# Performance work log

Hardware: AMD Instinct MI355X
Metric: run time of the kernel (lower is better)

## Reference

```python
import jax, jax.numpy as jnp
import numpy as np

N, M, K, C, FF, H, OUT = 20000, 80000, 48, 64, 256, 4, 64


def _lin(x, w, b):
    return x @ w.T + b


def _bn(x, g, b, eps=1e-5):
    mu = x.mean(0)
    var = x.var(0)
    return (x - mu) * jax.lax.rsqrt(var + eps) * g + b


def setup_inputs() -> dict:
    key = jax.random.key(0)
    ks = jax.random.split(key, 24)
    voxel_features = jax.random.normal(ks[0], (M, C), jnp.float32)
    voxel_coords = jax.random.normal(ks[1], (M, 3), jnp.float32)
    query_coords = jax.random.normal(ks[2], (N, 3), jnp.float32)
    idx = jax.random.randint(ks[3], (N, K), 0, M)
    drop = jax.random.uniform(ks[4], (N, K)) < 0.1
    drop = drop.at[:, 0].set(False)  # keep >=1 valid key per query
    key_indices = jnp.where(drop, -1, idx)
    s = 0.05
    p = lambda i, shp: jax.random.normal(ks[i], shp, jnp.float32) * s
    return {
        "voxel_features": voxel_features,
        "voxel_coords": voxel_coords,
        "query_coords": query_coords,
        "key_indices": key_indices,
        "q_w": p(5, (C, 3)), "q_b": p(6, (C,)),
        "kpos_w": p(7, (C, 3)), "kpos_b": p(8, (C,)),
        "in_w": p(9, (3 * C, C)), "in_b": p(10, (3 * C,)),
        "out_w": p(11, (C, C)), "out_b": p(12, (C,)),
        "lin1_w": p(13, (FF, C)), "lin1_b": p(14, (FF,)),
        "lin2_w": p(15, (C, FF)), "lin2_b": p(16, (C,)),
        "norm_g": jnp.ones((C,), jnp.float32), "norm_b": jnp.zeros((C,), jnp.float32),
        "outl_w": p(17, (OUT, C)), "outl_b": p(18, (OUT,)),
        "obn_g": jnp.ones((OUT,), jnp.float32), "obn_b": jnp.zeros((OUT,), jnp.float32),
    }


def reference(voxel_features, voxel_coords, query_coords, key_indices,
              q_w, q_b, kpos_w, kpos_b, in_w, in_b, out_w, out_b,
              lin1_w, lin1_b, lin2_w, lin2_b, norm_g, norm_b,
              outl_w, outl_b, obn_g, obn_b):
    hd = C // H
    mask = key_indices < 0                      # (N,K) padded keys
    safe = jnp.where(mask, 0, key_indices)
    key_feats = voxel_features[safe]            # (N,K,C) hash-gather
    key_coords = voxel_coords[safe]             # (N,K,3)
    # query positional projection
    q_feat = jax.nn.relu(_lin(query_coords, q_w, q_b))          # (N,C)
    # relative coords + key positional conv1d(kernel=1) == linear on coord dim
    rel = key_coords - query_coords[:, None, :]                  # (N,K,3)
    key_feats = key_feats + jax.nn.relu(_lin(rel, kpos_w, kpos_b))
    # multihead attention, query length 1 per voxel
    Wq, Wk, Wv = jnp.split(in_w, 3, axis=0)
    bq, bk, bv = jnp.split(in_b, 3)
    q = (_lin(q_feat, Wq, bq) / jnp.sqrt(jnp.float32(hd))).reshape(N, H, hd)
    k = _lin(key_feats, Wk, bk).reshape(N, K, H, hd)
    v = _lin(key_feats, Wv, bv).reshape(N, K, H, hd)
    scores = jnp.einsum('nhd,nkhd->nhk', q, k)
    scores = jnp.where(mask[:, None, :], -jnp.inf, scores)
    attn = jax.nn.softmax(scores, axis=-1)
    ctx = jnp.einsum('nhk,nkhd->nhd', attn, v).reshape(N, C)
    att = _lin(ctx, out_w, out_b)                                # (N,C)
    # FFN + residual
    x = att + _lin(jax.nn.relu(_lin(att, lin1_w, lin1_b)), lin2_w, lin2_b)
    x = _bn(x, norm_g, norm_b)
    # output layer: Linear -> BN -> ReLU
    x = jax.nn.relu(_bn(_lin(x, outl_w, outl_b), obn_g, obn_b))
    return x
```

## Files before the change

### kernel.cpp

```cpp
#include <hip/hip_runtime.h>
#include <math.h>

#define N_Q 20000
#define KK 48
#define CC 64
#define FFD 256

#define TW_WOT   0
#define TW_WVT   4096
#define TW_L1B   8192
#define TW_L2B   16384
#define TW_OLB   24576
#define TW_QB    26624
#define TW_KB    28672
#define ST_OFF   32768
#define M_OFF    33024
#define VF_OFF   2593024

typedef short bf16x8 __attribute__((ext_vector_type(8)));
typedef float f32x4  __attribute__((ext_vector_type(4)));

__device__ __forceinline__ unsigned f2bf(float f) {
    unsigned u = __float_as_uint(f);
    return (u + 0x7fffu + ((u >> 16) & 1u)) >> 16;
}
__device__ __forceinline__ unsigned pk2(float a, float b) {
    return f2bf(a) | (f2bf(b) << 16);
}
__device__ __forceinline__ float bflo(unsigned u) { return __uint_as_float(u << 16); }
__device__ __forceinline__ float bfhi(unsigned u) { return __uint_as_float(u & 0xffff0000u); }
__device__ __forceinline__ bf16x8 ldfrag(const unsigned short* p) {
    return *(const bf16x8*)p;
}

__global__ void prep_all(const float* __restrict__ in_w,
                         const float* __restrict__ out_w,
                         const float* __restrict__ lin1_w,
                         const float* __restrict__ lin2_w,
                         const float* __restrict__ outl_w,
                         const float* __restrict__ vfeat,
                         float* __restrict__ tw,
                         unsigned short* __restrict__ vfeat_bf,
                         float* __restrict__ stats)
{
    int t = blockIdx.x * 256 + threadIdx.x;
    unsigned* twu = (unsigned*)tw;
    if (t < 1280000) {
        float4 v = ((const float4*)vfeat)[t];
        uint2 p; p.x = pk2(v.x, v.y); p.y = pk2(v.z, v.w);
        ((uint2*)vfeat_bf)[t] = p;
    }
    if (t < 256) stats[t] = 0.0f;
    if (t < 4096) {
        int c = t >> 6, j = t & 63;
        tw[TW_WOT + j*64 + c] = out_w[c*64 + j];
    } else if (t < 8192) {
        if (t < 6144) {
            int p = t - 4096;
            int j2 = p & 3, lane = (p >> 2) & 63, nb = (p >> 8) & 3, ks = p >> 10;
            int nn = nb*16 + (lane & 15), k = ks*32 + (lane >> 4)*8 + 2*j2;
            twu[TW_WVT + p] = pk2(in_w[(128 + nn)*64 + k], in_w[(128 + nn)*64 + k + 1]);
        }
    } else if (t < 16384) {
        int p = t - 8192;
        int j2 = p & 3, lane = (p >> 2) & 63, nb = (p >> 8) & 15, ks = p >> 12;
        int n = nb*16 + (lane & 15), k = ks*32 + (lane >> 4)*8 + 2*j2;
        twu[TW_L1B + p] = pk2(lin1_w[n*64 + k], lin1_w[n*64 + k + 1]);
    } else if (t < 24576) {
        int p = t - 16384;
        int j2 = p & 3, lane = (p >> 2) & 63, nb = (p >> 8) & 3, ks = p >> 10;
        int n = nb*16 + (lane & 15), k = ks*32 + (lane >> 4)*8 + 2*j2;
        twu[TW_L2B + p] = pk2(lin2_w[n*256 + k], lin2_w[n*256 + k + 1]);
    } else if (t < 26624) {
        int p = t - 24576;
        int j2 = p & 3, lane = (p >> 2) & 63, nb = (p >> 8) & 3, ks = p >> 10;
        int n = nb*16 + (lane & 15), k = ks*32 + (lane >> 4)*8 + 2*j2;
        twu[TW_OLB + p] = pk2(outl_w[n*64 + k], outl_w[n*64 + k + 1]);
    } else if (t < 28672) {
        int p = t - 26624;
        int j2 = p & 3, lane = (p >> 2) & 63, nb = (p >> 8) & 3, ks = p >> 10;
        int n = nb*16 + (lane & 15), k = ks*32 + (lane >> 4)*8 + 2*j2;
        twu[TW_QB + p] = pk2(in_w[n*64 + k], in_w[n*64 + k + 1]);
    } else if (t < 32768) {
        int p = t - 28672;
        int j2 = p & 3, lane = (p >> 2) & 63, nb = (p >> 8) & 3, h = p >> 10;
        int j = nb*16 + (lane & 15), k = (lane >> 4)*8 + 2*j2;
        unsigned u = 0;
        if (k < 16)
            u = pk2(in_w[(64 + h*16 + k)*64 + j], in_w[(64 + h*16 + k + 1)*64 + j]);
        twu[TW_KB + p] = u;
    }
}

__global__ __launch_bounds__(256) void m_kernel(
    const float* __restrict__ qcoord, const float* __restrict__ q_w,
    const float* __restrict__ q_b, const float* __restrict__ in_b,
    const float* __restrict__ tw, unsigned short* __restrict__ M_all)
{
    __shared__ __align__(16) unsigned short sQF[80*72];
    __shared__ __align__(16) unsigned short sQ[80*72];
    int t = threadIdx.x, base = blockIdx.x * 80;
    int colq = (t*4) & 63;
    float qwv[12];
    #pragma unroll
    for (int j = 0; j < 12; ++j) qwv[j] = q_w[colq*3 + j];
    float4 qb4 = *(const float4*)&q_b[colq];
    #pragma unroll
    for (int i = 0; i < 5; ++i) {
        int e = i*1024 + t*4, r = e >> 6, n = base + r;
        float c0 = qcoord[n*3], c1 = qcoord[n*3+1], c2 = qcoord[n*3+2];
        float f0 = fmaxf(fmaf(qwv[2],  c2, fmaf(qwv[1],  c1, fmaf(qwv[0], c0, qb4.x))), 0.f);
        float f1 = fmaxf(fmaf(qwv[5],  c2, fmaf(qwv[4],  c1, fmaf(qwv[3], c0, qb4.y))), 0.f);
        float f2 = fmaxf(fmaf(qwv[8],  c2, fmaf(qwv[7],  c1, fmaf(qwv[6], c0, qb4.z))), 0.f);
        float f3 = fmaxf(fmaf(qwv[11], c2, fmaf(qwv[10], c1, fmaf(qwv[9], c0, qb4.w))), 0.f);
        uint2 p; p.x = pk2(f0, f1); p.y = pk2(f2, f3);
        *(uint2*)&sQF[r*72 + colq] = p;
    }
    int w = t >> 6, lane = t & 63, l16 = lane & 15, quad = lane >> 4;
    const unsigned* QB = (const unsigned*)(tw + TW_QB);
    const unsigned* KB = (const unsigned*)(tw + TW_KB);
    bf16x8 qbf[2], kbf[4];
    #pragma unroll
    for (int ks = 0; ks < 2; ++ks)
        qbf[ks] = ldfrag((const unsigned short*)&QB[((ks*4 + w)*64 + lane)*4]);
    #pragma unroll
    for (int nb = 0; nb < 4; ++nb)
        kbf[nb] = ldfrag((const unsigned short*)&KB[((w*4 + nb)*64 + lane)*4]);
    __syncthreads();

    int cq = w*16 + l16;
    float bq = in_b[cq];
    #pragma unroll
    for (int mb = 0; mb < 5; ++mb) {
        bf16x8 a0 = ldfrag(&sQF[(mb*16 + l16)*72 + quad*8]);
        bf16x8 a1 = ldfrag(&sQF[(mb*16 + l16)*72 + 32 + quad*8]);
        f32x4 acc = {0.f, 0.f, 0.f, 0.f};
        acc = __builtin_amdgcn_mfma_f32_16x16x32_bf16(a0, qbf[0], acc, 0, 0, 0);
        acc = __builtin_amdgcn_mfma_f32_16x16x32_bf16(a1, qbf[1], acc, 0, 0, 0);
        #pragma unroll
        for (int reg = 0; reg < 4; ++reg) {
            int row = mb*16 + quad*4 + reg;
            sQ[row*72 + cq] = (unsigned short)f2bf((acc[reg] + bq) * 0.25f);
        }
    }
    #pragma unroll
    for (int mb = 0; mb < 5; ++mb) {
        bf16x8 a = {0,0,0,0,0,0,0,0};
        if (quad < 2) a = ldfrag(&sQ[(mb*16 + l16)*72 + w*16 + quad*8]);
        f32x4 acc[4];
        #pragma unroll
        for (int nb = 0; nb < 4; ++nb) {
            f32x4 z = {0.f, 0.f, 0.f, 0.f};
            acc[nb] = __builtin_amdgcn_mfma_f32_16x16x32_bf16(a, kbf[nb], z, 0, 0, 0);
        }
        #pragma unroll
        for (int nb = 0; nb < 4; ++nb)
            #pragma unroll
            for (int reg = 0; reg < 4; ++reg) {
                int r = base + mb*16 + quad*4 + reg, j = nb*16 + l16;
                M_all[(size_t)r*256 + w*64 + j] = (unsigned short)f2bf(acc[nb][reg]);
            }
    }
}

__global__ __launch_bounds__(64, 4) void attn_kernel(
    const unsigned short* __restrict__ vfeat_bf, const float* __restrict__ vcoord,
    const float* __restrict__ qcoord, const int* __restrict__ kidx,
    const float* __restrict__ kpos_w, const float* __restrict__ kpos_b,
    const float* __restrict__ in_b, const float* __restrict__ out_b,
    const float* __restrict__ tw, const unsigned short* __restrict__ M_all,
    float* __restrict__ att_out)
{
    __shared__ __align__(16) unsigned short skf[KK*72];
    __shared__ __align__(16) float sctx[64];
    int n = blockIdx.x, c = threadIdx.x;
    int l16 = c & 15, quad = c >> 4;

    const unsigned short* Mrow = M_all + (size_t)n*256 + (l16 & 3)*64 + quad*8;
    bf16x8 mf0 = ldfrag(Mrow);
    bf16x8 mf1 = ldfrag(Mrow + 32);
    const unsigned* VBu = (const unsigned*)(tw + TW_WVT);
    bf16x8 wv[2][4];
    #pragma unroll
    for (int ks = 0; ks < 2; ++ks)
        #pragma unroll
        for (int nb = 0; nb < 4; ++nb)
            wv[ks][nb] = ldfrag((const unsigned short*)&VBu[((ks*4 + nb)*64 + c)*4]);

    float qc0 = qcoord[n*3+0], qc1 = qcoord[n*3+1], qc2 = qcoord[n*3+2];

    int kread = c < 48 ? c : 47;
    int idxv = kidx[(size_t)n*KK + kread];
    int sfe = idxv < 0 ? 0 : idxv;
    float rl0 = vcoord[sfe*3+0] - qc0;
    float rl1 = vcoord[sfe*3+1] - qc1;
    float rl2 = vcoord[sfe*3+2] - qc2;

    float4 wA  = *(const float4*)(kpos_w + 12*l16 + 0);
    float4 wB  = *(const float4*)(kpos_w + 12*l16 + 4);
    float4 wC  = *(const float4*)(kpos_w + 12*l16 + 8);
    float4 kb4 = *(const float4*)(kpos_b + 4*l16);

    uint2 fv[12];
    #pragma unroll
    for (int i = 0; i < 12; ++i) {
        int row = 4*i + quad;
        int si = __shfl(idxv, row);
        si = si < 0 ? 0 : si;
        fv[i] = *(const uint2*)(vfeat_bf + (size_t)si*64 + 4*l16);
    }
    #pragma unroll
    for (int i = 0; i < 12; ++i) {
        int row = 4*i + quad;
        float rr0 = __shfl(rl0, row), rr1 = __shfl(rl1, row), rr2 = __shfl(rl2, row);
        float g0 = bflo(fv[i].x), g1 = bfhi(fv[i].x);
        float g2 = bflo(fv[i].y), g3 = bfhi(fv[i].y);
        g0 += fmaxf(fmaf(wA.x, rr0, fmaf(wA.y, rr1, fmaf(wA.z, rr2, kb4.x))), 0.0f);
        g1 += fmaxf(fmaf(wA.w, rr0, fmaf(wB.x, rr1, fmaf(wB.y, rr2, kb4.y))), 0.0f);
        g2 += fmaxf(fmaf(wB.z, rr0, fmaf(wB.w, rr1, fmaf(wC.x, rr2, kb4.z))), 0.0f);
        g3 += fmaxf(fmaf(wC.y, rr0, fmaf(wC.z, rr1, fmaf(wC.w, rr2, kb4.w))), 0.0f);
        uint2 p; p.x = pk2(g0, g1); p.y = pk2(g2, g3);
        *(uint2*)&skf[row*72 + 4*l16] = p;
    }

    unsigned long long vm = __ballot(c < 48 && idxv >= 0);
    bf16x8 a0s[3], a1s[3];
    float S[3][4];
    #pragma unroll
    for (int mb = 0; mb < 3; ++mb) {
        a0s[mb] = ldfrag(&skf[(mb*16 + l16)*72 + quad*8]);
        a1s[mb] = ldfrag(&skf[(mb*16 + l16)*72 + 32 + quad*8]);
        f32x4 acc = {0.f, 0.f, 0.f, 0.f};
        acc = __builtin_amdgcn_mfma_f32_16x16x32_bf16(a0s[mb], mf0, acc, 0, 0, 0);
        acc = __builtin_amdgcn_mfma_f32_16x16x32_bf16(a1s[mb], mf1, acc, 0, 0, 0);
        #pragma unroll
        for (int r = 0; r < 4; ++r) {
            int kk = mb*16 + quad*4 + r;
            S[mb][r] = ((vm >> kk) & 1ull) ? acc[r] : -1e30f;
        }
    }

    float mx = S[0][0];
    #pragma unroll
    for (int mb = 0; mb < 3; ++mb)
        #pragma unroll
        for (int r = 0; r < 4; ++r) mx = fmaxf(mx, S[mb][r]);
    mx = fmaxf(mx, __shfl_xor(mx, 16));
    mx = fmaxf(mx, __shfl_xor(mx, 32));
    float p[3][4], es = 0.f;
    #pragma unroll
    for (int mb = 0; mb < 3; ++mb)
        #pragma unroll
        for (int r = 0; r < 4; ++r) { p[mb][r] = __expf(S[mb][r] - mx); es += p[mb][r]; }
    es += __shfl_xor(es, 16);
    es += __shfl_xor(es, 32);
    float rinv = 1.0f / es;
    #pragma unroll
    for (int mb = 0; mb < 3; ++mb)
        #pragma unroll
        for (int r = 0; r < 4; ++r) p[mb][r] *= rinv;

    float cacc0 = 0.f, cacc1 = 0.f, cacc2 = 0.f, cacc3 = 0.f;
    #pragma unroll
    for (int mb = 0; mb < 3; ++mb) {
        f32x4 av[4];
        #pragma unroll
        for (int nb = 0; nb < 4; ++nb) {
            f32x4 z = {0.f, 0.f, 0.f, 0.f};
            z = __builtin_amdgcn_mfma_f32_16x16x32_bf16(a0s[mb], wv[0][nb], z, 0, 0, 0);
            av[nb] = __builtin_amdgcn_mfma_f32_16x16x32_bf16(a1s[mb], wv[1][nb], z, 0, 0, 0);
        }
        #pragma unroll
        for (int r = 0; r < 4; ++r) {
            float pv = p[mb][r];
            float p0 = __shfl(pv, quad*16 + 0);
            float p1 = __shfl(pv, quad*16 + 1);
            float p2 = __shfl(pv, quad*16 + 2);
            float p3 = __shfl(pv, quad*16 + 3);
            cacc0 = fmaf(p0, av[0][r], cacc0);
            cacc1 = fmaf(p1, av[1][r], cacc1);
            cacc2 = fmaf(p2, av[2][r], cacc2);
            cacc3 = fmaf(p3, av[3][r], cacc3);
        }
    }
    cacc0 += __shfl_xor(cacc0, 16); cacc0 += __shfl_xor(cacc0, 32);
    cacc1 += __shfl_xor(cacc1, 16); cacc1 += __shfl_xor(cacc1, 32);
    cacc2 += __shfl_xor(cacc2, 16); cacc2 += __shfl_xor(cacc2, 32);
    cacc3 += __shfl_xor(cacc3, 16); cacc3 += __shfl_xor(cacc3, 32);
    float cv = quad == 0 ? cacc0 : quad == 1 ? cacc1 : quad == 2 ? cacc2 : cacc3;
    cv += in_b[128 + c];
    sctx[c] = cv;

    const float* WoT = tw + TW_WOT;
    float att = out_b[c];
    #pragma unroll 8
    for (int j = 0; j < 64; ++j)
        att = fmaf(sctx[j], WoT[j*64 + c], att);
    att_out[(size_t)n*64 + c] = att;
}

__global__ __launch_bounds__(256) void ffn_kernel(
    const float* __restrict__ tw, const float* __restrict__ lin1_b,
    const float* __restrict__ lin2_b, float* __restrict__ att_y,
    float* __restrict__ sum1, float* __restrict__ sumsq1)
{
    __shared__ __align__(16) unsigned short sA[80*72];
    __shared__ __align__(16) unsigned short sH[80*264];
    int t = threadIdx.x, base = blockIdx.x * 80;
    #pragma unroll
    for (int i = 0; i < 5; ++i) {
        int e = i*1024 + t*4, r = e >> 6, col = e & 63;
        float4 v = *(const float4*)&att_y[(size_t)(base + r)*64 + col];
        uint2 p; p.x = pk2(v.x, v.y); p.y = pk2(v.z, v.w);
        *(uint2*)&sA[r*72 + col] = p;
    }
    int w = t >> 6, lane = t & 63, l16 = lane & 15, quad = lane >> 4;
    const unsigned* L1B = (const unsigned*)(tw + TW_L1B);
    const unsigned* L2B = (const unsigned*)(tw + TW_L2B);
    bf16x8 b1f[2][4], b2f[8];
    #pragma unroll
    for (int ks = 0; ks < 2; ++ks)
        #pragma unroll
        for (int nb = 0; nb < 4; ++nb)
            b1f[ks][nb] = ldfrag((const unsigned short*)&L1B[((ks*16 + w*4 + nb)*64 + lane)*4]);
    #pragma unroll
    for (int ks = 0; ks < 8; ++ks)
        b2f[ks] = ldfrag((const unsigned short*)&L2B[((ks*4 + w)*64 + lane)*4]);
    __syncthreads();

    #pragma unroll
    for (int mb = 0; mb < 5; ++mb) {
        bf16x8 a0 = ldfrag(&sA[(mb*16 + l16)*72 + quad*8]);
        bf16x8 a1 = ldfrag(&sA[(mb*16 + l16)*72 + 32 + quad*8]);
        #pragma unroll
        for (int nb = 0; nb < 4; ++nb) {
            f32x4 acc = {0.f, 0.f, 0.f, 0.f};
            acc = __builtin_amdgcn_mfma_f32_16x16x32_bf16(a0, b1f[0][nb], acc, 0, 0, 0);
            acc = __builtin_amdgcn_mfma_f32_16x16x32_bf16(a1, b1f[1][nb], acc, 0, 0, 0);
            int f = w*64 + nb*16 + l16;
            float bias = lin1_b[f];
            #pragma unroll
            for (int reg = 0; reg < 4; ++reg) {
                int row = mb*16 + quad*4 + reg;
                sH[row*264 + f] = (unsigned short)f2bf(fmaxf(acc[reg] + bias, 0.0f));
            }
        }
    }
    __syncthreads();

    int c = w*16 + l16;
    float lb2 = lin2_b[c];
    float s = 0.f, ss = 0.f;
    #pragma unroll
    for (int mb = 0; mb < 5; ++mb) {
        f32x4 acc = {0.f, 0.f, 0.f, 0.f};
        #pragma unroll
        for (int ks = 0; ks < 8; ++ks) {
            bf16x8 a = ldfrag(&sH[(mb*16 + l16)*264 + ks*32 + quad*8]);
            acc = __builtin_amdgcn_mfma_f32_16x16x32_bf16(a, b2f[ks], acc, 0, 0, 0);
        }
        #pragma unroll
        for (int reg = 0; reg < 4; ++reg) {
            int r = base + mb*16 + quad*4 + reg;
            float y = att_y[(size_t)r*64 + c] + lb2 + acc[reg];
            att_y[(size_t)r*64 + c] = y;
            s += y; ss = fmaf(y, y, ss);
        }
    }
    s  += __shfl_xor(s, 16);  s  += __shfl_xor(s, 32);
    ss += __shfl_xor(ss, 16); ss += __shfl_xor(ss, 32);
    if (lane < 16) {
        atomicAdd(&sum1[c], s);
        atomicAdd(&sumsq1[c], ss);
    }
}

__global__ __launch_bounds__(256) void linout_kernel(
    const float* __restrict__ tw, const float* __restrict__ outl_b,
    const float* __restrict__ norm_g, const float* __restrict__ norm_b,
    const float* __restrict__ sum1, const float* __restrict__ sumsq1,
    const float* __restrict__ y, float* __restrict__ z_out,
    float* __restrict__ sum2, float* __restrict__ sumsq2)
{
    __shared__ __align__(16) unsigned short sX[80*72];
    int t = threadIdx.x, base = blockIdx.x * 80;
    int colq = (t*4) & 63;
    const float invN = 1.0f / 20000.0f;
    float4 sm = *(const float4*)&sum1[colq];
    float4 sq = *(const float4*)&sumsq1[colq];
    float4 g  = *(const float4*)&norm_g[colq];
    float4 bb = *(const float4*)&norm_b[colq];
    float mu0 = sm.x*invN, mu1 = sm.y*invN, mu2 = sm.z*invN, mu3 = sm.w*invN;
    float a0 = g.x / sqrtf(fmaf(-mu0, mu0, sq.x*invN) + 1e-5f);
    float a1 = g.y / sqrtf(fmaf(-mu1, mu1, sq.y*invN) + 1e-5f);
    float a2 = g.z / sqrtf(fmaf(-mu2, mu2, sq.z*invN) + 1e-5f);
    float a3 = g.w / sqrtf(fmaf(-mu3, mu3, sq.w*invN) + 1e-5f);
    float b0 = fmaf(-mu0, a0, bb.x), b1 = fmaf(-mu1, a1, bb.y);
    float b2 = fmaf(-mu2, a2, bb.z), b3 = fmaf(-mu3, a3, bb.w);
    #pragma unroll
    for (int i = 0; i < 5; ++i) {
        int e = i*1024 + t*4, r = e >> 6;
        float4 v = *(const float4*)&y[(size_t)(base + r)*64 + colq];
        uint2 p;
        p.x = pk2(fmaf(v.x, a0, b0), fmaf(v.y, a1, b1));
        p.y = pk2(fmaf(v.z, a2, b2), fmaf(v.w, a3, b3));
        *(uint2*)&sX[r*72 + colq] = p;
    }
    int w = t >> 6, lane = t & 63, l16 = lane & 15, quad = lane >> 4;
    const unsigned* OLB = (const unsigned*)(tw + TW_OLB);
    bf16x8 obf[2];
    #pragma unroll
    for (int ks = 0; ks < 2; ++ks)
        obf[ks] = ldfrag((const unsigned short*)&OLB[((ks*4 + w)*64 + lane)*4]);
    __syncthreads();

    int co = w*16 + l16;
    float ob = outl_b[co];
    float s = 0.f, ss = 0.f;
    #pragma unroll
    for (int mb = 0; mb < 5; ++mb) {
        bf16x8 x0 = ldfrag(&sX[(mb*16 + l16)*72 + quad*8]);
        bf16x8 x1 = ldfrag(&sX[(mb*16 + l16)*72 + 32 + quad*8]);
        f32x4 acc = {0.f, 0.f, 0.f, 0.f};
        acc = __builtin_amdgcn_mfma_f32_16x16x32_bf16(x0, obf[0], acc, 0, 0, 0);
        acc = __builtin_amdgcn_mfma_f32_16x16x32_bf16(x1, obf[1], acc, 0, 0, 0);
        #pragma unroll
        for (int reg = 0; reg < 4; ++reg) {
            int r = base + mb*16 + quad*4 + reg;
            float zv = acc[reg] + ob;
            z_out[(size_t)r*64 + co] = zv;
            s += zv; ss = fmaf(zv, zv, ss);
        }
    }
    s  += __shfl_xor(s, 16);  s  += __shfl_xor(s, 32);
    ss += __shfl_xor(ss, 16); ss += __shfl_xor(ss, 32);
    if (lane < 16) {
        atomicAdd(&sum2[co], s);
        atomicAdd(&sumsq2[co], ss);
    }
}

__global__ void final_kernel(float* __restrict__ z,
    const float* __restrict__ sum2, const float* __restrict__ sumsq2,
    const float* __restrict__ obn_g, const float* __restrict__ obn_b)
{
    int i = blockIdx.x*blockDim.x + threadIdx.x;
    if (i >= N_Q*64/4) return;
    int o4 = (i*4) & 63;
    float4 sm = *(const float4*)&sum2[o4];
    float4 sq = *(const float4*)&sumsq2[o4];
    float4 g  = *(const float4*)&obn_g[o4];
    float4 b  = *(const float4*)&obn_b[o4];
    const float invN = 1.0f / 20000.0f;
    float mux = sm.x*invN, muy = sm.y*invN, muz = sm.z*invN, muw = sm.w*invN;
    float ax = g.x / sqrtf(fmaf(-mux, mux, sq.x*invN) + 1e-5f);
    float ay = g.y / sqrtf(fmaf(-muy, muy, sq.y*invN) + 1e-5f);
    float az = g.z / sqrtf(fmaf(-muz, muz, sq.z*invN) + 1e-5f);
    float aw = g.w / sqrtf(fmaf(-muw, muw, sq.w*invN) + 1e-5f);
    float4 v = ((float4*)z)[i];
    v.x = fmaxf(fmaf(v.x - mux, ax, b.x), 0.0f);
    v.y = fmaxf(fmaf(v.y - muy, ay, b.y), 0.0f);
    v.z = fmaxf(fmaf(v.z - muz, az, b.z), 0.0f);
    v.w = fmaxf(fmaf(v.w - muw, aw, b.w), 0.0f);
    ((float4*)z)[i] = v;
}

extern "C" void kernel_launch(void* const* d_in, const int* in_sizes, int n_in,
                              void* d_out, int out_size, void* d_ws, size_t ws_size,
                              hipStream_t stream)
{
    const float* vfeat  = (const float*)d_in[0];
    const float* vcoord = (const float*)d_in[1];
    const float* qcoord = (const float*)d_in[2];
    const int*   kidx   = (const int*)d_in[3];
    const float* q_w    = (const float*)d_in[4];
    const float* q_b    = (const float*)d_in[5];
    const float* kpos_w = (const float*)d_in[6];
    const float* kpos_b = (const float*)d_in[7];
    const float* in_w   = (const float*)d_in[8];
    const float* in_b   = (const float*)d_in[9];
    const float* out_w  = (const float*)d_in[10];
    const float* out_b  = (const float*)d_in[11];
    const float* lin1_w = (const float*)d_in[12];
    const float* lin1_b = (const float*)d_in[13];
    const float* lin2_w = (const float*)d_in[14];
    const float* lin2_b = (const float*)d_in[15];
    const float* norm_g = (const float*)d_in[16];
    const float* norm_b = (const float*)d_in[17];
    const float* outl_w = (const float*)d_in[18];
    const float* outl_b = (const float*)d_in[19];
    const float* obn_g  = (const float*)d_in[20];
    const float* obn_b  = (const float*)d_in[21];

    float* ws = (float*)d_ws;
    float* tw = ws;
    float* stats = ws + ST_OFF;
    float* sum1 = stats, *sumsq1 = stats + 64, *sum2 = stats + 128, *sumsq2 = stats + 192;
    unsigned short* M_all = (unsigned short*)(ws + M_OFF);
    unsigned short* vfeat_bf = (unsigned short*)(ws + VF_OFF);
    float* xd = (float*)d_out;

    prep_all<<<5120, 256, 0, stream>>>(in_w, out_w, lin1_w, lin2_w, outl_w,
                                       vfeat, tw, vfeat_bf, stats);
    m_kernel<<<250, 256, 0, stream>>>(qcoord, q_w, q_b, in_b, tw, M_all);
    attn_kernel<<<N_Q, 64, 0, stream>>>(vfeat_bf, vcoord, qcoord, kidx, kpos_w, kpos_b,
                                        in_b, out_b, tw, M_all, xd);
    ffn_kernel<<<250, 256, 0, stream>>>(tw, lin1_b, lin2_b, xd, sum1, sumsq1);
    linout_kernel<<<250, 256, 0, stream>>>(tw, outl_b, norm_g, norm_b, sum1, sumsq1,
                                           xd, xd, sum2, sumsq2);
    final_kernel<<<1250, 256, 0, stream>>>(xd, sum2, sumsq2, obn_g, obn_b);
}
```

Before: 185.6 us.

## Move out-projection into FFN kernel as MFMA GEMM and pack two queries per attn block

The per-query scalar out_proj loop (64x64 FMAs reading a transposed fp32 weight) is removed from the attention kernel. The attention kernel now writes ctx, and the FFN kernel runs out_proj as a bf16 MFMA GEMM over 80-row tiles, keeping att in registers for the residual. The attention kernel also handles two queries per 128-thread block, halving the block count. This trades fp32 precision on out_proj for bf16 and adds LDS reuse of the sH buffer in the FFN kernel.

```diff
diff --git a/kernel.cpp b/kernel.cpp
--- a/kernel.cpp
+++ b/kernel.cpp
@@ -6,7 +6,7 @@
 #define CC 64
 #define FFD 256
 
-#define TW_WOT   0
+#define TW_WOB   0
 #define TW_WVT   4096
 #define TW_L1B   8192
 #define TW_L2B   16384
@@ -52,8 +52,12 @@
     }
     if (t < 256) stats[t] = 0.0f;
     if (t < 4096) {
-        int c = t >> 6, j = t & 63;
-        tw[TW_WOT + j*64 + c] = out_w[c*64 + j];
+        if (t < 2048) {
+            int p = t;
+            int j2 = p & 3, lane = (p >> 2) & 63, nb = (p >> 8) & 3, ks = p >> 10;
+            int nn = nb*16 + (lane & 15), k = ks*32 + (lane >> 4)*8 + 2*j2;
+            twu[TW_WOB + p] = pk2(out_w[nn*64 + k], out_w[nn*64 + k + 1]);
+        }
     } else if (t < 8192) {
         if (t < 6144) {
             int p = t - 4096;
@@ -163,29 +167,30 @@
     }
 }
 
-__global__ __launch_bounds__(64, 4) void attn_kernel(
+__global__ __launch_bounds__(128, 4) void attn_kernel(
     const unsigned short* __restrict__ vfeat_bf, const float* __restrict__ vcoord,
     const float* __restrict__ qcoord, const int* __restrict__ kidx,
     const float* __restrict__ kpos_w, const float* __restrict__ kpos_b,
-    const float* __restrict__ in_b, const float* __restrict__ out_b,
+    const float* __restrict__ in_b,
     const float* __restrict__ tw, const unsigned short* __restrict__ M_all,
-    float* __restrict__ att_out)
-{
-    __shared__ __align__(16) unsigned short skf[KK*72];
-    __shared__ __align__(16) float sctx[64];
-    int n = blockIdx.x, c = threadIdx.x;
+    float* __restrict__ ctx_out)
+{
+    __shared__ __align__(16) unsigned short skf2[2][KK*72];
+    int wv = threadIdx.x >> 6, c = threadIdx.x & 63;
+    int n = blockIdx.x * 2 + wv;
+    unsigned short* skf = skf2[wv];
     int l16 = c & 15, quad = c >> 4;
 
     const unsigned short* Mrow = M_all + (size_t)n*256 + (l16 & 3)*64 + quad*8;
     bf16x8 mf0 = ldfrag(Mrow);
     bf16x8 mf1 = ldfrag(Mrow + 32);
     const unsigned* VBu = (const unsigned*)(tw + TW_WVT);
-    bf16x8 wv[2][4];
+    bf16x8 wvf[2][4];
     #pragma unroll
     for (int ks = 0; ks < 2; ++ks)
         #pragma unroll
         for (int nb = 0; nb < 4; ++nb)
-            wv[ks][nb] = ldfrag((const unsigned short*)&VBu[((ks*4 + nb)*64 + c)*4]);
+            wvf[ks][nb] = ldfrag((const unsigned short*)&VBu[((ks*4 + nb)*64 + c)*4]);
 
     float qc0 = qcoord[n*3+0], qc1 = qcoord[n*3+1], qc2 = qcoord[n*3+2];
 
@@ -267,8 +272,8 @@
         #pragma unroll
         for (int nb = 0; nb < 4; ++nb) {
             f32x4 z = {0.f, 0.f, 0.f, 0.f};
-            z = __builtin_amdgcn_mfma_f32_16x16x32_bf16(a0s[mb], wv[0][nb], z, 0, 0, 0);
-            av[nb] = __builtin_amdgcn_mfma_f32_16x16x32_bf16(a1s[mb], wv[1][nb], z, 0, 0, 0);
+            z = __builtin_amdgcn_mfma_f32_16x16x32_bf16(a0s[mb], wvf[0][nb], z, 0, 0, 0);
+            av[nb] = __builtin_amdgcn_mfma_f32_16x16x32_bf16(a1s[mb], wvf[1][nb], z, 0, 0, 0);
         }
         #pragma unroll
         for (int r = 0; r < 4; ++r) {
@@ -289,35 +294,34 @@
     cacc3 += __shfl_xor(cacc3, 16); cacc3 += __shfl_xor(cacc3, 32);
     float cv = quad == 0 ? cacc0 : quad == 1 ? cacc1 : quad == 2 ? cacc2 : cacc3;
     cv += in_b[128 + c];
-    sctx[c] = cv;
-
-    const float* WoT = tw + TW_WOT;
-    float att = out_b[c];
-    #pragma unroll 8
-    for (int j = 0; j < 64; ++j)
-        att = fmaf(sctx[j], WoT[j*64 + c], att);
-    att_out[(size_t)n*64 + c] = att;
+    ctx_out[(size_t)n*64 + c] = cv;
 }
 
 __global__ __launch_bounds__(256) void ffn_kernel(
-    const float* __restrict__ tw, const float* __restrict__ lin1_b,
-    const float* __restrict__ lin2_b, float* __restrict__ att_y,
+    const float* __restrict__ tw, const float* __restrict__ out_b,
+    const float* __restrict__ lin1_b, const float* __restrict__ lin2_b,
+    float* __restrict__ ctx_y,
     float* __restrict__ sum1, float* __restrict__ sumsq1)
 {
     __shared__ __align__(16) unsigned short sA[80*72];
     __shared__ __align__(16) unsigned short sH[80*264];
+    unsigned short* sC = sH;
     int t = threadIdx.x, base = blockIdx.x * 80;
     #pragma unroll
     for (int i = 0; i < 5; ++i) {
         int e = i*1024 + t*4, r = e >> 6, col = e & 63;
-        float4 v = *(const float4*)&att_y[(size_t)(base + r)*64 + col];
+        float4 v = *(const float4*)&ctx_y[(size_t)(base + r)*64 + col];
         uint2 p; p.x = pk2(v.x, v.y); p.y = pk2(v.z, v.w);
-        *(uint2*)&sA[r*72 + col] = p;
+        *(uint2*)&sC[r*72 + col] = p;
     }
     int w = t >> 6, lane = t & 63, l16 = lane & 15, quad = lane >> 4;
+    const unsigned* WOB = (const unsigned*)(tw + TW_WOB);
     const unsigned* L1B = (const unsigned*)(tw + TW_L1B);
     const unsigned* L2B = (const unsigned*)(tw + TW_L2B);
-    bf16x8 b1f[2][4], b2f[8];
+    bf16x8 wob[2], b1f[2][4], b2f[8];
+    #pragma unroll
+    for (int ks = 0; ks < 2; ++ks)
+        wob[ks] = ldfrag((const unsigned short*)&WOB[((ks*4 + w)*64 + lane)*4]);
     #pragma unroll
     for (int ks = 0; ks < 2; ++ks)
         #pragma unroll
@@ -326,6 +330,26 @@
     #pragma unroll
     for (int ks = 0; ks < 8; ++ks)
         b2f[ks] = ldfrag((const unsigned short*)&L2B[((ks*4 + w)*64 + lane)*4]);
+    __syncthreads();
+
+    int c = w*16 + l16;
+    float ob = out_b[c];
+    f32x4 attacc[5];
+    #pragma unroll
+    for (int mb = 0; mb < 5; ++mb) {
+        bf16x8 a0 = ldfrag(&sC[(mb*16 + l16)*72 + quad*8]);
+        bf16x8 a1 = ldfrag(&sC[(mb*16 + l16)*72 + 32 + quad*8]);
+        f32x4 acc = {0.f, 0.f, 0.f, 0.f};
+        acc = __builtin_amdgcn_mfma_f32_16x16x32_bf16(a0, wob[0], acc, 0, 0, 0);
+        acc = __builtin_amdgcn_mfma_f32_16x16x32_bf16(a1, wob[1], acc, 0, 0, 0);
+        #pragma unroll
+        for (int reg = 0; reg < 4; ++reg) {
+            float av = acc[reg] + ob;
+            attacc[mb][reg] = av;
+            int row = mb*16 + quad*4 + reg;
+            sA[row*72 + c] = (unsigned short)f2bf(av);
+        }
+    }
     __syncthreads();
 
     #pragma unroll
@@ -348,7 +372,6 @@
     }
     __syncthreads();
 
-    int c = w*16 + l16;
     float lb2 = lin2_b[c];
     float s = 0.f, ss = 0.f;
     #pragma unroll
@@ -362,8 +385,8 @@
         #pragma unroll
         for (int reg = 0; reg < 4; ++reg) {
             int r = base + mb*16 + quad*4 + reg;
-            float y = att_y[(size_t)r*64 + c] + lb2 + acc[reg];
-            att_y[(size_t)r*64 + c] = y;
+            float y = attacc[mb][reg] + lb2 + acc[reg];
+            ctx_y[(size_t)r*64 + c] = y;
             s += y; ss = fmaf(y, y, ss);
         }
     }
@@ -503,9 +526,9 @@
     prep_all<<<5120, 256, 0, stream>>>(in_w, out_w, lin1_w, lin2_w, outl_w,
                                        vfeat, tw, vfeat_bf, stats);
     m_kernel<<<250, 256, 0, stream>>>(qcoord, q_w, q_b, in_b, tw, M_all);
-    attn_kernel<<<N_Q, 64, 0, stream>>>(vfeat_bf, vcoord, qcoord, kidx, kpos_w, kpos_b,
-                                        in_b, out_b, tw, M_all, xd);
-    ffn_kernel<<<250, 256, 0, stream>>>(tw, lin1_b, lin2_b, xd, sum1, sumsq1);
+    attn_kernel<<<N_Q/2, 128, 0, stream>>>(vfeat_bf, vcoord, qcoord, kidx, kpos_w,
+                                           kpos_b, in_b, tw, M_all, xd);
+    ffn_kernel<<<250, 256, 0, stream>>>(tw, out_b, lin1_b, lin2_b, xd, sum1, sumsq1);
     linout_kernel<<<250, 256, 0, stream>>>(tw, outl_b, norm_g, norm_b, sum1, sumsq1,
                                            xd, xd, sum2, sumsq2);
     final_kernel<<<1250, 256, 0, stream>>>(xd, sum2, sumsq2, obn_g, obn_b);
```

After: 179.2 us. 3.4% less time.
